# Kernel tuning notes

Hardware: AMD Instinct MI355X
Metric: run time of the kernel (lower is better)

## Reference

```python
import jax, jax.numpy as jnp
import numpy as np

DEPTH = 3  # args.depth (chemprop default)


def setup_inputs() -> dict:
    key = jax.random.key(0)
    ks = jax.random.split(key, 10)
    n_atoms, n_bonds, max_nb, n_mols = 100000, 200000, 6, 4000
    H, AF, BF = 300, 133, 147  # hidden_size, atom_fdim, bond_fdim

    f_atoms = jax.random.normal(ks[0], (n_atoms, AF), jnp.float32)
    f_bonds = jax.random.normal(ks[1], (n_bonds, BF), jnp.float32)
    a2b = jax.random.randint(ks[2], (n_atoms, max_nb), 0, n_bonds)      # incoming bonds per atom
    b2a = jax.random.randint(ks[3], (n_bonds,), 0, n_atoms)             # source atom per bond
    b2revb = jax.random.randint(ks[4], (n_bonds,), 0, n_bonds)          # reverse bond index
    atom_mol = jnp.sort(jax.random.randint(ks[5], (n_atoms,), 0, n_mols))  # contiguous mol segments (a_scope)

    # Learned params (W_i, W_h bias-free per args.bias=False; W_o has bias)
    W_i = jax.random.normal(ks[6], (BF, H), jnp.float32) * (1.0 / np.sqrt(BF))
    W_h = jax.random.normal(ks[7], (H, H), jnp.float32) * (1.0 / np.sqrt(H))
    W_o = jax.random.normal(ks[8], (AF + H, H), jnp.float32) * (1.0 / np.sqrt(AF + H))
    b_o = jax.random.normal(ks[9], (H,), jnp.float32) * 0.01

    return dict(f_atoms=f_atoms, f_bonds=f_bonds, W_i=W_i, W_h=W_h, W_o=W_o, b_o=b_o,
                a2b=a2b, b2a=b2a, b2revb=b2revb, atom_mol=atom_mol, n_mols=n_mols)


def reference(f_atoms, f_bonds, W_i, W_h, W_o, b_o, a2b, b2a, b2revb, atom_mol, n_mols):
    # Bond-message D-MPNN (atom_messages=False), ReLU activation, dropout=0 (eval)
    inp = f_bonds @ W_i                       # [n_bonds, H]
    message = jax.nn.relu(inp)
    for _ in range(DEPTH - 1):
        nei_a_message = message[a2b]          # [n_atoms, max_nb, H] gather
        a_message = nei_a_message.sum(axis=1) # [n_atoms, H]
        message = a_message[b2a] - message[b2revb]  # [n_bonds, H]
        message = jax.nn.relu(inp + message @ W_h)
    # Atom readout
    a_message = message[a2b].sum(axis=1)      # [n_atoms, H]
    a_input = jnp.concatenate([f_atoms, a_message], axis=1)
    atom_hiddens = jax.nn.relu(a_input @ W_o + b_o)  # [n_atoms, H]
    # Per-molecule mean aggregation (a_scope loop -> segment ops)
    sums = jax.ops.segment_sum(atom_hiddens, atom_mol, num_segments=n_mols)
    counts = jax.ops.segment_sum(jnp.ones((atom_hiddens.shape[0],), atom_hiddens.dtype),
                                 atom_mol, num_segments=n_mols)
    return sums / jnp.maximum(counts, 1.0)[:, None]  # empty mols -> zero vector
```

## Files before the change

### kernel.cpp

```cpp
#include <hip/hip_runtime.h>
#include <hip/hip_bf16.h>
#include <stdint.h>


#define H_DIM 300
#define HP 320
#define AF_DIM 133
#define BF_DIM 147
#define MAXNB 6

typedef __hip_bfloat16 bf16;
typedef __attribute__((ext_vector_type(8))) short short8;
typedef __attribute__((ext_vector_type(4))) float f32x4;

__device__ __forceinline__ float b2f_raw(unsigned short u) {
    union { unsigned int i; float f; } v; v.i = ((unsigned int)u) << 16; return v.f;
}
__device__ __forceinline__ unsigned short f2b_raw(float f) {
    union { float f; unsigned int i; } v; v.f = f;
    unsigned int x = v.i;
    x += 0x7fffu + ((x >> 16) & 1u);
    return (unsigned short)(x >> 16);
}

__global__ __launch_bounds__(256) void prep_wt(
    const float* __restrict__ s1, int r1,
    const float* __restrict__ s2, int r2,
    unsigned short* __restrict__ Wt, int nkt)
{
    const int Ktot = nkt * 32;
    const int idx = blockIdx.x * 256 + threadIdx.x;
    if (idx >= 320 * Ktot) return;
    const int n = idx % 320;
    const int k = idx / 320;
    float v = 0.f;
    if (n < H_DIM) {
        if (k < 320) { if (k < r1) v = s1[k * H_DIM + n]; }
        else { const int kk = k - 320; if (kk < r2) v = s2[kk * H_DIM + n]; }
    }
    Wt[n * Ktot + k] = f2b_raw(v);
}

template <int MODE, bool RELU_A>
__global__ __launch_bounds__(256) void mfma_gemm(
    const bf16* __restrict__ Ab,
    const float* __restrict__ Afp,
    const unsigned short* __restrict__ Wt,
    const float* __restrict__ bias,
    bf16* __restrict__ out,
    int M)
{
    constexpr int NKT  = (MODE == 1) ? 5 : (MODE == 4 ? 10 : 15);
    constexpr int KTOT = NKT * 32;
    constexpr int FPW  = (MODE == 3) ? AF_DIM : BF_DIM;
    constexpr bool RELU_OUT = (MODE == 3);

    __shared__ char As[2][64 * 64];
    __shared__ char Cs[16 * 640];

    const int t    = threadIdx.x;
    const int m0   = blockIdx.x * 64;
    const int wave = t >> 6;
    const int lane = t & 63;
    const int l16  = lane & 15;
    const int quad = lane >> 4;
    const int swz  = ((quad ^ (l16 & 3)) << 4);

    const int am  = t >> 2;
    const int c   = t & 3;
    const int gm  = m0 + am;
    const bool mok = (gm < M);
    const int aoff = am * 64 + ((c ^ (am & 3)) << 4);

    auto load_a = [&](int kt) -> uint4 {
        uint4 aval = {0u, 0u, 0u, 0u};
        if (!mok) return aval;
        if (MODE == 1) {
            const int k = kt * 32 + c * 8;
            unsigned short* rp = (unsigned short*)&aval;
#pragma unroll
            for (int j = 0; j < 8; ++j) {
                const int kk = k + j;
                rp[j] = (kk < BF_DIM) ? f2b_raw(Afp[(long)gm * BF_DIM + kk]) : 0;
            }
        } else if (MODE == 4 || kt < 10) {
            const int k = kt * 32 + c * 8;
            aval = *(const uint4*)((const char*)Ab + ((long)gm * HP + k) * 2);
            if (RELU_A) {
                unsigned short* rp = (unsigned short*)&aval;
#pragma unroll
                for (int j = 0; j < 8; ++j)
                    rp[j] = (rp[j] & 0x8000u) ? 0 : rp[j];
            }
        } else {
            const int k2 = (kt - 10) * 32 + c * 8;
            unsigned short* rp = (unsigned short*)&aval;
#pragma unroll
            for (int j = 0; j < 8; ++j) {
                const int kk = k2 + j;
                rp[j] = (kk < FPW) ? f2b_raw(Afp[(long)gm * FPW + kk]) : 0;
            }
        }
        return aval;
    };

    auto load_b = [&](int kt, short8* bfr) {
        const int kbase = kt * 32 + quad * 8;
#pragma unroll
        for (int nt = 0; nt < 5; ++nt) {
            const int nn = wave * 80 + nt * 16 + l16;
            bfr[nt] = *(const short8*)(Wt + (long)nn * KTOT + kbase);
        }
    };

    f32x4 acc[4][5];
#pragma unroll
    for (int i = 0; i < 4; ++i)
#pragma unroll
        for (int j = 0; j < 5; ++j) acc[i][j] = (f32x4){0.f, 0.f, 0.f, 0.f};

    uint4 aval = load_a(0);
    *(uint4*)(As[0] + aoff) = aval;
    short8 bfr[5];
    load_b(0, bfr);

    for (int kt = 0; kt < NKT; ++kt) {
        short8 bfr_n[5];
        if (kt + 1 < NKT) {
            aval = load_a(kt + 1);
            load_b(kt + 1, bfr_n);
        }
        __syncthreads();
        short8 afr[4];
#pragma unroll
        for (int mt = 0; mt < 4; ++mt)
            afr[mt] = *(const short8*)(As[kt & 1] + mt * 1024 + l16 * 64 + swz);
#pragma unroll
        for (int nt = 0; nt < 5; ++nt)
#pragma unroll
            for (int mt = 0; mt < 4; ++mt)
                acc[mt][nt] = __builtin_amdgcn_mfma_f32_16x16x32_bf16(
                    afr[mt], bfr[nt], acc[mt][nt], 0, 0, 0);
        if (kt + 1 < NKT) {
            *(uint4*)(As[(kt + 1) & 1] + aoff) = aval;
#pragma unroll
            for (int nt = 0; nt < 5; ++nt) bfr[nt] = bfr_n[nt];
        }
    }

    for (int mt = 0; mt < 4; ++mt) {
        __syncthreads();
#pragma unroll
        for (int nt = 0; nt < 5; ++nt) {
            const int col = wave * 80 + nt * 16 + l16;
            float bv = 0.f;
            if (MODE == 3) bv = (col < H_DIM) ? bias[col] : 0.f;
#pragma unroll
            for (int r = 0; r < 4; ++r) {
                float v = acc[mt][nt][r] + bv;
                if (RELU_OUT) v = fmaxf(v, 0.f);
                ((unsigned short*)Cs)[(quad * 4 + r) * HP + col] = f2b_raw(v);
            }
        }
        __syncthreads();
        const int gr0 = m0 + mt * 16;
#pragma unroll
        for (int i = 0; i < 3; ++i) {
            const int idx = i * 256 + t;
            if (idx < 640) {
                const int row = idx / 40;
                if (gr0 + row < M)
                    *(uint4*)((char*)out + (long)(gr0 + row) * 640 + (idx - row * 40) * 16)
                        = *(const uint4*)(Cs + idx * 16);
            }
        }
    }
}

__global__ __launch_bounds__(256) void gather_sum_kernel(
    const bf16* __restrict__ msg, const int* __restrict__ a2b,
    bf16* __restrict__ amsg, int n_atoms)
{
    const int idx = blockIdx.x * 256 + threadIdx.x;
    if (idx >= n_atoms * (HP / 8)) return;
    const int a = idx / (HP / 8);
    const int cc = idx - a * (HP / 8);
    float s[8] = {0.f, 0.f, 0.f, 0.f, 0.f, 0.f, 0.f, 0.f};
    const int base = a * MAXNB;
#pragma unroll
    for (int j = 0; j < MAXNB; ++j) {
        const long b = a2b[base + j];
        const uint4 u = *(const uint4*)((const char*)msg + (b * HP + cc * 8) * 2);
        const unsigned short* up = (const unsigned short*)&u;
#pragma unroll
        for (int e = 0; e < 8; ++e) s[e] += b2f_raw(up[e]);
    }
    uint4 r;
    unsigned short* rp = (unsigned short*)&r;
#pragma unroll
    for (int e = 0; e < 8; ++e) rp[e] = f2b_raw(s[e]);
    *(uint4*)((char*)amsg + ((long)a * HP + cc * 8) * 2) = r;
}

__global__ __launch_bounds__(256) void combine_kernel(
    const bf16* __restrict__ inp, const bf16* __restrict__ Gh,
    const bf16* __restrict__ Hm, const int* __restrict__ b2a,
    const int* __restrict__ b2revb, bf16* __restrict__ outm, int n_bonds)
{
    const int idx = blockIdx.x * 256 + threadIdx.x;
    if (idx >= n_bonds * (HP / 8)) return;
    const int b = idx / (HP / 8);
    const int cc = idx - b * (HP / 8);
    const long co = (long)cc * 16;
    const long ra = b2a[b];
    const long rb = b2revb[b];
    const uint4 vi = *(const uint4*)((const char*)inp + (long)b * 640 + co);
    const uint4 vg = *(const uint4*)((const char*)Gh + ra * 640 + co);
    const uint4 vh = *(const uint4*)((const char*)Hm + rb * 640 + co);
    const unsigned short* ip = (const unsigned short*)&vi;
    const unsigned short* gp = (const unsigned short*)&vg;
    const unsigned short* hp = (const unsigned short*)&vh;
    uint4 r;
    unsigned short* rp = (unsigned short*)&r;
#pragma unroll
    for (int e = 0; e < 8; ++e) {
        const float v = b2f_raw(ip[e]) + b2f_raw(gp[e]) - b2f_raw(hp[e]);
        rp[e] = f2b_raw(fmaxf(v, 0.f));
    }
    *(uint4*)((char*)outm + (long)b * 640 + co) = r;
}

__global__ __launch_bounds__(256) void seg_mean_kernel(
    const bf16* __restrict__ hidden, const int* __restrict__ atom_mol,
    float* __restrict__ out, int n_atoms)
{
    const int m = blockIdx.x;
    __shared__ int s_lo, s_hi;
    if (threadIdx.x == 0) {
        int lo = 0, hi = n_atoms;
        while (lo < hi) { int mid = (lo + hi) >> 1; if (atom_mol[mid] < m) lo = mid + 1; else hi = mid; }
        s_lo = lo;
        int lo2 = lo; hi = n_atoms;
        while (lo2 < hi) { int mid = (lo2 + hi) >> 1; if (atom_mol[mid] < m + 1) lo2 = mid + 1; else hi = mid; }
        s_hi = lo2;
    }
    __syncthreads();
    const int lo = s_lo, hi = s_hi;
    const float inv = 1.0f / (float)max(hi - lo, 1);
    for (int cpass = 0; cpass < 2; ++cpass) {
        const int c = cpass * 256 + threadIdx.x;
        if (c >= H_DIM) break;
        float s = 0.f;
        for (int a = lo; a < hi; ++a)
            s += b2f_raw(((const unsigned short*)hidden)[(long)a * HP + c]);
        out[(long)m * H_DIM + c] = s * inv;
    }
}

extern "C" void kernel_launch(void* const* d_in, const int* in_sizes, int n_in,
                              void* d_out, int out_size, void* d_ws, size_t ws_size,
                              hipStream_t stream)
{
    const float* f_atoms = (const float*)d_in[0];
    const float* f_bonds = (const float*)d_in[1];
    const float* W_i     = (const float*)d_in[2];
    const float* W_h     = (const float*)d_in[3];
    const float* W_o     = (const float*)d_in[4];
    const float* b_o     = (const float*)d_in[5];
    const int*  a2b      = (const int*)d_in[6];
    const int*  b2a      = (const int*)d_in[7];
    const int*  b2revb   = (const int*)d_in[8];
    const int*  atom_mol = (const int*)d_in[9];

    const int n_atoms = in_sizes[0] / AF_DIM;
    const int n_bonds = in_sizes[1] / BF_DIM;
    const int n_mols  = out_size / H_DIM;

    char* ws = (char*)d_ws;
    size_t off = 0;
    auto alloc = [&](size_t bytes) {
        size_t o = off; off += (bytes + 255) & ~(size_t)255; return o;
    };
    bf16* inpB = (bf16*)(ws + alloc((size_t)n_bonds * HP * 2));
    bf16* msgX = (bf16*)(ws + alloc((size_t)n_bonds * HP * 2));
    bf16* HmB  = (bf16*)(ws + alloc((size_t)n_bonds * HP * 2));
    bf16* amsg = (bf16*)(ws + alloc((size_t)n_atoms * HP * 2));
    unsigned short* Wt1 = (unsigned short*)(ws + alloc(320 * 160 * 2));
    unsigned short* WtH = (unsigned short*)(ws + alloc(320 * 320 * 2));
    unsigned short* Wt3 = (unsigned short*)(ws + alloc(320 * 480 * 2));
    bf16* hidden = HmB;

    const dim3 blk(256);

    prep_wt<<<(320 * 160 + 255) / 256, blk, 0, stream>>>(W_i, BF_DIM, nullptr, 0, Wt1, 5);
    prep_wt<<<(320 * 320 + 255) / 256, blk, 0, stream>>>(W_h, H_DIM, nullptr, 0, WtH, 10);
    prep_wt<<<(320 * 480 + 255) / 256, blk, 0, stream>>>(W_o + (size_t)AF_DIM * H_DIM, H_DIM,
                                                         W_o, AF_DIM, Wt3, 15);

    const int gB = (n_bonds + 63) / 64;
    const int gA = (n_atoms + 63) / 64;
    const int gG = (n_atoms * (HP / 8) + 255) / 256;
    const int gC = (n_bonds * (HP / 8) + 255) / 256;

    mfma_gemm<1, false><<<gB, blk, 0, stream>>>(nullptr, f_bonds, Wt1, nullptr, inpB, n_bonds);

    mfma_gemm<4, true><<<gB, blk, 0, stream>>>(inpB, nullptr, WtH, nullptr, HmB, n_bonds);
    gather_sum_kernel<<<gG, blk, 0, stream>>>(HmB, a2b, amsg, n_atoms);
    combine_kernel<<<gC, blk, 0, stream>>>(inpB, amsg, HmB, b2a, b2revb, msgX, n_bonds);

    mfma_gemm<4, false><<<gB, blk, 0, stream>>>(msgX, nullptr, WtH, nullptr, HmB, n_bonds);
    gather_sum_kernel<<<gG, blk, 0, stream>>>(HmB, a2b, amsg, n_atoms);
    combine_kernel<<<gC, blk, 0, stream>>>(inpB, amsg, HmB, b2a, b2revb, msgX, n_bonds);

    gather_sum_kernel<<<gG, blk, 0, stream>>>(msgX, a2b, amsg, n_atoms);
    mfma_gemm<3, false><<<gA, blk, 0, stream>>>(amsg, f_atoms, Wt3, b_o, hidden, n_atoms);

    seg_mean_kernel<<<n_mols, blk, 0, stream>>>(hidden, atom_mol, (float*)d_out, n_atoms);
}
```

Measured before the change: 960.6 us.

## Pre-convert fp32 inputs to padded bf16 and widen GEMM blocks to 8 waves

```diff
diff --git a/kernel.cpp b/kernel.cpp
--- a/kernel.cpp
+++ b/kernel.cpp
@@ -12,6 +12,7 @@
 typedef __hip_bfloat16 bf16;
 typedef __attribute__((ext_vector_type(8))) short short8;
 typedef __attribute__((ext_vector_type(4))) float f32x4;
+typedef __attribute__((ext_vector_type(2))) unsigned int uint2v;
 
 __device__ __forceinline__ float b2f_raw(unsigned short u) {
     union { unsigned int i; float f; } v; v.i = ((unsigned int)u) << 16; return v.f;
@@ -41,19 +42,33 @@
     Wt[n * Ktot + k] = f2b_raw(v);
 }
 
-template <int MODE, bool RELU_A>
-__global__ __launch_bounds__(256) void mfma_gemm(
-    const bf16* __restrict__ Ab,
-    const float* __restrict__ Afp,
+__global__ __launch_bounds__(256) void prep_cvt(
+    const float* __restrict__ in, int W,
+    unsigned short* __restrict__ outb, int ostride, int M)
+{
+    const int idx = blockIdx.x * 256 + threadIdx.x;
+    if (idx >= M * 20) return;
+    const int r = idx / 20;
+    const int cc = idx - r * 20;
+    uint4 o;
+    unsigned short* op = (unsigned short*)&o;
+#pragma unroll
+    for (int j = 0; j < 8; ++j) {
+        const int k = cc * 8 + j;
+        op[j] = (k < W) ? f2b_raw(in[(long)r * W + k]) : 0;
+    }
+    *(uint4*)(outb + (long)r * ostride + cc * 8) = o;
+}
+
+template <int NKT, int ASTRIDE, bool RELU_A, bool BIAS_RELU>
+__global__ __launch_bounds__(512) void mfma_gemm(
+    const unsigned short* __restrict__ Ab,
     const unsigned short* __restrict__ Wt,
     const float* __restrict__ bias,
     bf16* __restrict__ out,
     int M)
 {
-    constexpr int NKT  = (MODE == 1) ? 5 : (MODE == 4 ? 10 : 15);
     constexpr int KTOT = NKT * 32;
-    constexpr int FPW  = (MODE == 3) ? AF_DIM : BF_DIM;
-    constexpr bool RELU_OUT = (MODE == 3);
 
     __shared__ char As[2][64 * 64];
     __shared__ char Cs[16 * 640];
@@ -61,66 +76,50 @@
     const int t    = threadIdx.x;
     const int m0   = blockIdx.x * 64;
     const int wave = t >> 6;
+    const int wr   = wave & 1;
+    const int wc   = wave >> 1;
     const int lane = t & 63;
     const int l16  = lane & 15;
     const int quad = lane >> 4;
     const int swz  = ((quad ^ (l16 & 3)) << 4);
 
-    const int am  = t >> 2;
-    const int c   = t & 3;
+    const int am  = t >> 3;
+    const int c   = t & 7;
     const int gm  = m0 + am;
     const bool mok = (gm < M);
-    const int aoff = am * 64 + ((c ^ (am & 3)) << 4);
-
-    auto load_a = [&](int kt) -> uint4 {
-        uint4 aval = {0u, 0u, 0u, 0u};
-        if (!mok) return aval;
-        if (MODE == 1) {
-            const int k = kt * 32 + c * 8;
-            unsigned short* rp = (unsigned short*)&aval;
-#pragma unroll
-            for (int j = 0; j < 8; ++j) {
-                const int kk = k + j;
-                rp[j] = (kk < BF_DIM) ? f2b_raw(Afp[(long)gm * BF_DIM + kk]) : 0;
-            }
-        } else if (MODE == 4 || kt < 10) {
-            const int k = kt * 32 + c * 8;
-            aval = *(const uint4*)((const char*)Ab + ((long)gm * HP + k) * 2);
+    const int aoff = am * 64 + (((c >> 1) ^ (am & 3)) << 4) + (c & 1) * 8;
+
+    auto load_a = [&](int kt) -> uint2v {
+        uint2v v = {0u, 0u};
+        if (mok) {
+            v = *(const uint2v*)((const char*)Ab + (long)gm * ASTRIDE + kt * 64 + c * 8);
             if (RELU_A) {
-                unsigned short* rp = (unsigned short*)&aval;
-#pragma unroll
-                for (int j = 0; j < 8; ++j)
+                unsigned short* rp = (unsigned short*)&v;
+#pragma unroll
+                for (int j = 0; j < 4; ++j)
                     rp[j] = (rp[j] & 0x8000u) ? 0 : rp[j];
             }
-        } else {
-            const int k2 = (kt - 10) * 32 + c * 8;
-            unsigned short* rp = (unsigned short*)&aval;
-#pragma unroll
-            for (int j = 0; j < 8; ++j) {
-                const int kk = k2 + j;
-                rp[j] = (kk < FPW) ? f2b_raw(Afp[(long)gm * FPW + kk]) : 0;
-            }
-        }
-        return aval;
+        }
+        return v;
     };
 
     auto load_b = [&](int kt, short8* bfr) {
         const int kbase = kt * 32 + quad * 8;
 #pragma unroll
         for (int nt = 0; nt < 5; ++nt) {
-            const int nn = wave * 80 + nt * 16 + l16;
+            const int nn = wc * 80 + nt * 16 + l16;
             bfr[nt] = *(const short8*)(Wt + (long)nn * KTOT + kbase);
         }
     };
 
-    f32x4 acc[4][5];
-#pragma unroll
-    for (int i = 0; i < 4; ++i)
+    f32x4 acc[2][5];
+#pragma unroll
+    for (int i = 0; i < 2; ++i)
 #pragma unroll
         for (int j = 0; j < 5; ++j) acc[i][j] = (f32x4){0.f, 0.f, 0.f, 0.f};
 
-    uint4 aval = load_a(0);
-    *(uint4*)(As[0] + aoff) = aval;
+    uint2v aval = load_a(0);
+    *(uint2v*)(As[0] + aoff) = aval;
     short8 bfr[5];
     load_b(0, bfr);
 
@@ -131,42 +130,45 @@
             load_b(kt + 1, bfr_n);
         }
         __syncthreads();
-        short8 afr[4];
-#pragma unroll
-        for (int mt = 0; mt < 4; ++mt)
-            afr[mt] = *(const short8*)(As[kt & 1] + mt * 1024 + l16 * 64 + swz);
+        short8 afr[2];
+#pragma unroll
+        for (int mt = 0; mt < 2; ++mt)
+            afr[mt] = *(const short8*)(As[kt & 1] + (wr * 32 + mt * 16 + l16) * 64 + swz);
 #pragma unroll
         for (int nt = 0; nt < 5; ++nt)
 #pragma unroll
-            for (int mt = 0; mt < 4; ++mt)
+            for (int mt = 0; mt < 2; ++mt)
                 acc[mt][nt] = __builtin_amdgcn_mfma_f32_16x16x32_bf16(
                     afr[mt], bfr[nt], acc[mt][nt], 0, 0, 0);
         if (kt + 1 < NKT) {
-            *(uint4*)(As[(kt + 1) & 1] + aoff) = aval;
+            *(uint2v*)(As[(kt + 1) & 1] + aoff) = aval;
 #pragma unroll
             for (int nt = 0; nt < 5; ++nt) bfr[nt] = bfr_n[nt];
         }
     }
 
-    for (int mt = 0; mt < 4; ++mt) {
+    for (int s = 0; s < 4; ++s) {
         __syncthreads();
-#pragma unroll
-        for (int nt = 0; nt < 5; ++nt) {
-            const int col = wave * 80 + nt * 16 + l16;
-            float bv = 0.f;
-            if (MODE == 3) bv = (col < H_DIM) ? bias[col] : 0.f;
-#pragma unroll
-            for (int r = 0; r < 4; ++r) {
-                float v = acc[mt][nt][r] + bv;
-                if (RELU_OUT) v = fmaxf(v, 0.f);
-                ((unsigned short*)Cs)[(quad * 4 + r) * HP + col] = f2b_raw(v);
+        if (wr == (s >> 1)) {
+            const int mt = s & 1;
+#pragma unroll
+            for (int nt = 0; nt < 5; ++nt) {
+                const int col = wc * 80 + nt * 16 + l16;
+                float bv = 0.f;
+                if (BIAS_RELU) bv = (col < H_DIM) ? bias[col] : 0.f;
+#pragma unroll
+                for (int r = 0; r < 4; ++r) {
+                    float v = acc[mt][nt][r] + bv;
+                    if (BIAS_RELU) v = fmaxf(v, 0.f);
+                    ((unsigned short*)Cs)[(quad * 4 + r) * HP + col] = f2b_raw(v);
+                }
             }
         }
         __syncthreads();
-        const int gr0 = m0 + mt * 16;
-#pragma unroll
-        for (int i = 0; i < 3; ++i) {
-            const int idx = i * 256 + t;
+        const int gr0 = m0 + s * 16;
+#pragma unroll
+        for (int i = 0; i < 2; ++i) {
+            const int idx = i * 512 + t;
             if (idx < 640) {
                 const int row = idx / 40;
                 if (gr0 + row < M)
@@ -179,7 +181,7 @@
 
 __global__ __launch_bounds__(256) void gather_sum_kernel(
     const bf16* __restrict__ msg, const int* __restrict__ a2b,
-    bf16* __restrict__ amsg, int n_atoms)
+    unsigned short* __restrict__ amsg, int ostride, int n_atoms)
 {
     const int idx = blockIdx.x * 256 + threadIdx.x;
     if (idx >= n_atoms * (HP / 8)) return;
@@ -199,7 +201,7 @@
     unsigned short* rp = (unsigned short*)&r;
 #pragma unroll
     for (int e = 0; e < 8; ++e) rp[e] = f2b_raw(s[e]);
-    *(uint4*)((char*)amsg + ((long)a * HP + cc * 8) * 2) = r;
+    *(uint4*)(amsg + (long)a * ostride + cc * 8) = r;
 }
 
 __global__ __launch_bounds__(256) void combine_kernel(
@@ -288,9 +290,11 @@
     unsigned short* Wt1 = (unsigned short*)(ws + alloc(320 * 160 * 2));
     unsigned short* WtH = (unsigned short*)(ws + alloc(320 * 320 * 2));
     unsigned short* Wt3 = (unsigned short*)(ws + alloc(320 * 480 * 2));
+    unsigned short* fb16    = (unsigned short*)HmB;
+    unsigned short* atomcat = (unsigned short*)inpB;
     bf16* hidden = HmB;
 
-    const dim3 blk(256);
+    const dim3 blk(256), blkg(512);
 
     prep_wt<<<(320 * 160 + 255) / 256, blk, 0, stream>>>(W_i, BF_DIM, nullptr, 0, Wt1, 5);
     prep_wt<<<(320 * 320 + 255) / 256, blk, 0, stream>>>(W_h, H_DIM, nullptr, 0, WtH, 10);
@@ -302,18 +306,23 @@
     const int gG = (n_atoms * (HP / 8) + 255) / 256;
     const int gC = (n_bonds * (HP / 8) + 255) / 256;
 
-    mfma_gemm<1, false><<<gB, blk, 0, stream>>>(nullptr, f_bonds, Wt1, nullptr, inpB, n_bonds);
-
-    mfma_gemm<4, true><<<gB, blk, 0, stream>>>(inpB, nullptr, WtH, nullptr, HmB, n_bonds);
-    gather_sum_kernel<<<gG, blk, 0, stream>>>(HmB, a2b, amsg, n_atoms);
+    prep_cvt<<<(n_bonds * 20 + 255) / 256, blk, 0, stream>>>(f_bonds, BF_DIM, fb16, 160, n_bonds);
+
+    mfma_gemm<5, 320, false, false><<<gB, blkg, 0, stream>>>(fb16, Wt1, nullptr, inpB, n_bonds);
+
+    mfma_gemm<10, 640, true, false><<<gB, blkg, 0, stream>>>(
+        (const unsigned short*)inpB, WtH, nullptr, HmB, n_bonds);
+    gather_sum_kernel<<<gG, blk, 0, stream>>>(HmB, a2b, (unsigned short*)amsg, HP, n_atoms);
     combine_kernel<<<gC, blk, 0, stream>>>(inpB, amsg, HmB, b2a, b2revb, msgX, n_bonds);
 
-    mfma_gemm<4, false><<<gB, blk, 0, stream>>>(msgX, nullptr, WtH, nullptr, HmB, n_bonds);
-    gather_sum_kernel<<<gG, blk, 0, stream>>>(HmB, a2b, amsg, n_atoms);
+    mfma_gemm<10, 640, false, false><<<gB, blkg, 0, stream>>>(
+        (const unsigned short*)msgX, WtH, nullptr, HmB, n_bonds);
+    gather_sum_kernel<<<gG, blk, 0, stream>>>(HmB, a2b, (unsigned short*)amsg, HP, n_atoms);
     combine_kernel<<<gC, blk, 0, stream>>>(inpB, amsg, HmB, b2a, b2revb, msgX, n_bonds);
 
-    gather_sum_kernel<<<gG, blk, 0, stream>>>(msgX, a2b, amsg, n_atoms);
-    mfma_gemm<3, false><<<gA, blk, 0, stream>>>(amsg, f_atoms, Wt3, b_o, hidden, n_atoms);
+    prep_cvt<<<(n_atoms * 20 + 255) / 256, blk, 0, stream>>>(f_atoms, AF_DIM, atomcat + 320, 480, n_atoms);
+    gather_sum_kernel<<<gG, blk, 0, stream>>>(msgX, a2b, atomcat, 480, n_atoms);
+    mfma_gemm<15, 960, false, true><<<gA, blkg, 0, stream>>>(atomcat, Wt3, b_o, hidden, n_atoms);
 
     seg_mean_kernel<<<n_mols, blk, 0, stream>>>(hidden, atom_mol, (float*)d_out, n_atoms);
 }
```

Measured after the change: 1.245 ms. +29.6%, slower.
